# Kernel optimization log

Hardware: AMD Instinct MI355X
Metric: run time of the kernel (lower is better)

## Reference

```python
import jax, jax.numpy as jnp
import numpy as np

# config (matches init_kwargs)
B, L, Q = 4, 2048, 2048      # batch, memory_length, query_len
H, D = 16, 64                # heads, head_dim
E = H * D                    # hidden_dim = 1024
NB = 512                     # num_basis
SIGMAS = np.array([0.005, 0.01])
RIDGE = 0.5
CLAMP_MIN = 1e-4


def _build_basis():
    # torch.meshgrid(linspace(0,1,NB//2), sigmas) then flatten: mu repeated, sigma tiled
    mu = np.repeat(np.linspace(0.0, 1.0, NB // len(SIGMAS)), len(SIGMAS))
    sg = np.tile(SIGMAS, NB // len(SIGMAS))
    return mu, sg


def _build_G(mu, sg):
    # get_positions(L, padding=True), L even: 2L points in [-0.5+shift, 1.5-shift]
    shift = 1.0 / (2 * L)
    pos = np.linspace(-0.5 + shift, 1.5 - shift, 2 * L)
    # F[j, p] = N(pos_p; mu_j, sg_j)
    Fm = np.exp(-0.5 * ((pos[None, :] - mu[:, None]) / sg[:, None]) ** 2) / (sg[:, None] * np.sqrt(2 * np.pi))
    G = Fm.T @ np.linalg.inv(Fm @ Fm.T + RIDGE * np.eye(NB))  # [2L, NB]
    return G[L // 2:-(L // 2)]  # [L, NB]


def setup_inputs() -> dict:
    key = jax.random.key(0)
    ks = jax.random.split(key, 8)
    mu, sg = _build_basis()
    G = _build_G(mu, sg)
    s_e = 1.0 / np.sqrt(E)
    s_n = 1.0 / np.sqrt(NB)
    return {
        "k": jax.random.normal(ks[0], (B, L, E), jnp.float32),
        "q": jax.random.normal(ks[1], (B, Q, E), jnp.float32),
        "Wq": jax.random.normal(ks[2], (E, E), jnp.float32) * s_e,
        "Wk": jax.random.normal(ks[3], (E, E), jnp.float32) * s_e,
        "Wv": jax.random.normal(ks[4], (E, E), jnp.float32) * s_e,
        "Wo": jax.random.normal(ks[5], (E, E), jnp.float32) * s_e,
        "w_mu": jax.random.normal(ks[6], (NB,), jnp.float32) * s_n,
        "w_sigma": jax.random.normal(ks[7], (NB,), jnp.float32) * s_n,
        "Gs": jnp.asarray(G, jnp.float32),
        "basis_mu": jnp.asarray(mu, jnp.float32),
        "basis_sigma": jnp.asarray(sg, jnp.float32),
    }


def reference(k, q, Wq, Wk, Wv, Wo, w_mu, w_sigma, Gs, basis_mu, basis_sigma):
    # continuous compression of the memory: B_mat[b,n,e] = sum_l k[b,l,e] * Gs[l,n]
    Bm = jnp.einsum('ble,ln->bne', k, Gs)  # [B, NB, E]
    keys = (Bm @ Wk.T).reshape(B, NB, H, D).transpose(0, 2, 1, 3)   # [B,H,NB,D]
    vals = (Bm @ Wv.T).reshape(B, NB, H, D).transpose(0, 2, 1, 3)   # [B,H,NB,D]
    qry = (q @ Wq.T).reshape(B, Q, H, D).transpose(0, 2, 1, 3)      # [B,H,Q,D]
    # scores over basis functions
    scores = jnp.einsum('bhqd,bhnd->bhqn', qry, keys) / jnp.sqrt(jnp.float32(D))
    # affine heads -> Gaussian attention density parameters per query
    mu_q = jax.nn.sigmoid(scores @ w_mu)[..., None]                         # [B,H,Q,1]
    sig2 = jnp.clip(jax.nn.softplus(scores @ w_sigma), CLAMP_MIN)[..., None]  # [B,H,Q,1]
    # continuous softmax closed form: r_j = N(mu_q; basis_mu_j, sig2 + basis_sigma_j^2)
    var = sig2 + basis_sigma ** 2                                           # [B,H,Q,NB]
    r = jnp.exp(-0.5 * (mu_q - basis_mu) ** 2 / var) / jnp.sqrt(2.0 * jnp.pi * var)
    ctx = jnp.einsum('bhqn,bhnd->bhqd', r, vals)                            # [B,H,Q,D]
    ctx = ctx.transpose(0, 2, 1, 3).reshape(B, Q, E)
    return ctx @ Wo.T
```

## Files before the change

kernel.cpp:

```cpp
#include <hip/hip_runtime.h>

#define BB 4
#define LL 2048
#define QQ 2048
#define HH 16
#define DD 64
#define EE 1024
#define NB 512

typedef __attribute__((ext_vector_type(8))) short bf16x8;
typedef __attribute__((ext_vector_type(4))) float f32x4;

__device__ inline ushort bf16_rne(float f) {
  uint u = __float_as_uint(f);
  return (ushort)((u + 0x7fffu + ((u >> 16) & 1u)) >> 16);
}
__device__ inline float bf16_f(ushort h) { return __uint_as_float((uint)h << 16); }
__device__ inline void hilo(float x, ushort& h, ushort& l) {
  h = bf16_rne(x);
  l = bf16_rne(x - bf16_f(h));
}

__device__ inline void cvt8_pack(const float* a, uint4& ph, uint4& pl) {
  ushort h[8], l[8];
  #pragma unroll
  for (int j = 0; j < 8; j++) hilo(a[j], h[j], l[j]);
  ph = make_uint4((uint)h[0] | ((uint)h[1] << 16), (uint)h[2] | ((uint)h[3] << 16),
                  (uint)h[4] | ((uint)h[5] << 16), (uint)h[6] | ((uint)h[7] << 16));
  pl = make_uint4((uint)l[0] | ((uint)l[1] << 16), (uint)l[2] | ((uint)l[3] << 16),
                  (uint)l[4] | ((uint)l[5] << 16), (uint)l[6] | ((uint)l[7] << 16));
}

__device__ inline void xcd_remap(int& bx, int& by, int& bz) {
  int gx = gridDim.x, gy = gridDim.y;
  int nwg = gx * gy * (int)gridDim.z;
  int lin = blockIdx.x + gx * (blockIdx.y + gy * blockIdx.z);
  int swz = (lin & 7) * (nwg >> 3) + (lin >> 3);
  bx = swz % gx; int tmp = swz / gx; by = tmp % gy; bz = tmp / gy;
}

__global__ __launch_bounds__(256) void cvt_hilo(
    const float* __restrict__ x, ushort* __restrict__ hi, ushort* __restrict__ lo, long n)
{
  long i0 = ((long)blockIdx.x * 256 + threadIdx.x) * 8;
  long stride = (long)gridDim.x * 2048;
  for (long i = i0; i < n; i += stride) {
    float a[8];
    *(float4*)&a[0] = *(const float4*)&x[i];
    *(float4*)&a[4] = *(const float4*)&x[i + 4];
    uint4 ph, pl;
    cvt8_pack(a, ph, pl);
    *(uint4*)&hi[i] = ph;
    *(uint4*)&lo[i] = pl;
  }
}

__global__ __launch_bounds__(256) void cvt_hilo2(
    const float* __restrict__ x0, ushort* __restrict__ h0, ushort* __restrict__ l0,
    const float* __restrict__ x1, ushort* __restrict__ h1, ushort* __restrict__ l1, long n)
{
  const float* x = blockIdx.y ? x1 : x0;
  ushort* hi = blockIdx.y ? h1 : h0;
  ushort* lo = blockIdx.y ? l1 : l0;
  long i0 = ((long)blockIdx.x * 256 + threadIdx.x) * 8;
  long stride = (long)gridDim.x * 2048;
  for (long i = i0; i < n; i += stride) {
    float a[8];
    *(float4*)&a[0] = *(const float4*)&x[i];
    *(float4*)&a[4] = *(const float4*)&x[i + 4];
    uint4 ph, pl;
    cvt8_pack(a, ph, pl);
    *(uint4*)&hi[i] = ph;
    *(uint4*)&lo[i] = pl;
  }
}

__global__ __launch_bounds__(256) void cvt_hiloT(
    const float* __restrict__ x, ushort* __restrict__ hiT, ushort* __restrict__ loT,
    int R, int C, long zIn, long zOut)
{
  x += (long)blockIdx.z * zIn; hiT += (long)blockIdx.z * zOut; loT += (long)blockIdx.z * zOut;
  __shared__ float tile[32][33];
  const int t = threadIdx.x;
  const long r0 = (long)blockIdx.y * 32, c0 = (long)blockIdx.x * 32;
  {
    int row = t >> 3, c4 = t & 7;
    float4 v = *(const float4*)&x[(r0 + row) * C + c0 + c4 * 4];
    tile[row][c4*4+0] = v.x; tile[row][c4*4+1] = v.y;
    tile[row][c4*4+2] = v.z; tile[row][c4*4+3] = v.w;
  }
  __syncthreads();
  {
    int col = t >> 3, r4 = t & 7;
    ushort h[4], l[4];
    #pragma unroll
    for (int j = 0; j < 4; j++) hilo(tile[r4 * 4 + j][col], h[j], l[j]);
    uint2 ph = make_uint2((uint)h[0] | ((uint)h[1] << 16), (uint)h[2] | ((uint)h[3] << 16));
    uint2 pl = make_uint2((uint)l[0] | ((uint)l[1] << 16), (uint)l[2] | ((uint)l[3] << 16));
    long o = (c0 + col) * (long)R + r0 + r4 * 4;
    *(uint2*)&hiT[o] = ph;
    *(uint2*)&loT[o] = pl;
  }
}

__global__ __launch_bounds__(256) void add_pairs(
    float* __restrict__ dst, long dstStride,
    const float* __restrict__ src, long srcPairStride, long n)
{
  float* d = dst + (long)blockIdx.z * dstStride;
  const float* s0 = src + (long)blockIdx.z * srcPairStride;
  const float* s1 = s0 + n;
  long i0 = ((long)blockIdx.x * 256 + threadIdx.x) * 4;
  long stride = (long)gridDim.x * 1024;
  for (long i = i0; i < n; i += stride) {
    float4 a = *(const float4*)&s0[i];
    float4 b = *(const float4*)&s1[i];
    a.x += b.x; a.y += b.y; a.z += b.z; a.w += b.w;
    *(float4*)&d[i] = a;
  }
}


__global__ __launch_bounds__(256) void gemm_nt128(
    const float* __restrict__ A, const float* __restrict__ B, float* __restrict__ C,
    int N, int K, long sA, long sB, long sC, int NS, int Kc)
{
  const int z = blockIdx.z;
  const int b = z / NS, ks = z - b * NS;
  A += (long)b * sA + (long)ks * Kc;
  B += (long)b * sB + (long)ks * Kc;
  C += (long)z * sC;
  __shared__ float As[32][132], Bs[32][132];
  const int t = threadIdx.x;
  const int tx = t & 15, ty = t >> 4;
  const long m0 = (long)blockIdx.y * 128, n0 = (long)blockIdx.x * 128;
  float acc[8][8] = {};
  for (int k0 = 0; k0 < Kc; k0 += 32) {
    #pragma unroll
    for (int i = 0; i < 4; i++) {
      int f = t + i * 256;
      int r = f >> 3, k4 = f & 7;
      float4 va = *(const float4*)&A[(m0 + r) * K + k0 + k4 * 4];
      As[k4*4+0][r] = va.x; As[k4*4+1][r] = va.y; As[k4*4+2][r] = va.z; As[k4*4+3][r] = va.w;
      float4 vb = *(const float4*)&B[(n0 + r) * K + k0 + k4 * 4];
      Bs[k4*4+0][r] = vb.x; Bs[k4*4+1][r] = vb.y; Bs[k4*4+2][r] = vb.z; Bs[k4*4+3][r] = vb.w;
    }
    __syncthreads();
    #pragma unroll
    for (int kk = 0; kk < 32; kk++) {
      float4 a0 = *(const float4*)&As[kk][ty*8];
      float4 a1 = *(const float4*)&As[kk][ty*8+4];
      float4 b0 = *(const float4*)&Bs[kk][tx*8];
      float4 b1 = *(const float4*)&Bs[kk][tx*8+4];
      float ar[8] = {a0.x,a0.y,a0.z,a0.w,a1.x,a1.y,a1.z,a1.w};
      float br[8] = {b0.x,b0.y,b0.z,b0.w,b1.x,b1.y,b1.z,b1.w};
      #pragma unroll
      for (int i = 0; i < 8; i++)
        #pragma unroll
        for (int j = 0; j < 8; j++)
          acc[i][j] += ar[i] * br[j];
    }
    __syncthreads();
  }
  #pragma unroll
  for (int i = 0; i < 8; i++) {
    float4 o0 = make_float4(acc[i][0], acc[i][1], acc[i][2], acc[i][3]);
    float4 o1 = make_float4(acc[i][4], acc[i][5], acc[i][6], acc[i][7]);
    *(float4*)&C[(m0 + ty*8 + i) * N + n0 + tx*8    ] = o0;
    *(float4*)&C[(m0 + ty*8 + i) * N + n0 + tx*8 + 4] = o1;
  }
}

__global__ __launch_bounds__(256) void gemm_tn128(
    const float* __restrict__ A, const float* __restrict__ B, float* __restrict__ C,
    int M, int N, long sA, long sB, long sC, int NS, int Kc)
{
  const int z = blockIdx.z;
  const int b = z / NS, ks = z - b * NS;
  A += (long)b * sA + (long)ks * Kc * M;
  B += (long)b * sB + (long)ks * Kc * N;
  C += (long)z * sC;
  __shared__ float As[32][132], Bs[32][132];
  const int t = threadIdx.x;
  const int tx = t & 15, ty = t >> 4;
  const long m0 = (long)blockIdx.y * 128, n0 = (long)blockIdx.x * 128;
  float acc[8][8] = {};
  for (int k0 = 0; k0 < Kc; k0 += 32) {
    #pragma unroll
    for (int i = 0; i < 4; i++) {
      int f = t + i * 256;
      int r = f >> 5, c4 = f & 31;
      *(float4*)&As[r][c4 * 4] = *(const float4*)&A[(long)(k0 + r) * M + m0 + c4 * 4];
      *(float4*)&Bs[r][c4 * 4] = *(const float4*)&B[(long)(k0 + r) * N + n0 + c4 * 4];
    }
    __syncthreads();
    #pragma unroll
    for (int kk = 0; kk < 32; kk++) {
      float4 a0 = *(const float4*)&As[kk][ty*8];
      float4 a1 = *(const float4*)&As[kk][ty*8+4];
      float4 b0 = *(const float4*)&Bs[kk][tx*8];
      float4 b1 = *(const float4*)&Bs[kk][tx*8+4];
      float ar[8] = {a0.x,a0.y,a0.z,a0.w,a1.x,a1.y,a1.z,a1.w};
      float br[8] = {b0.x,b0.y,b0.z,b0.w,b1.x,b1.y,b1.z,b1.w};
      #pragma unroll
      for (int i = 0; i < 8; i++)
        #pragma unroll
        for (int j = 0; j < 8; j++)
          acc[i][j] += ar[i] * br[j];
    }
    __syncthreads();
  }
  #pragma unroll
  for (int i = 0; i < 8; i++) {
    float4 o0 = make_float4(acc[i][0], acc[i][1], acc[i][2], acc[i][3]);
    float4 o1 = make_float4(acc[i][4], acc[i][5], acc[i][6], acc[i][7]);
    *(float4*)&C[(m0 + ty*8 + i) * N + n0 + tx*8    ] = o0;
    *(float4*)&C[(m0 + ty*8 + i) * N + n0 + tx*8 + 4] = o1;
  }
}

__global__ __launch_bounds__(256) void gemm_nt64(
    const float* __restrict__ A, const float* __restrict__ B, float* __restrict__ C,
    int M, int N, int K, long sA, long sB, long sC)
{
  A += (long)blockIdx.z * sA; B += (long)blockIdx.z * sB; C += (long)blockIdx.z * sC;
  __shared__ float As[32][68], Bs[32][68];
  const int t = threadIdx.x;
  const int tx = t & 15, ty = t >> 4;
  const int m0 = blockIdx.y * 64, n0 = blockIdx.x * 64;
  float acc[4][4] = {};
  for (int k0 = 0; k0 < K; k0 += 32) {
    #pragma unroll
    for (int i = 0; i < 2; i++) {
      int f = t + i * 256;
      int r = f >> 3, k4 = f & 7;
      float4 va = *(const float4*)&A[(long)(m0 + r) * K + k0 + k4 * 4];
      As[k4*4+0][r] = va.x; As[k4*4+1][r] = va.y; As[k4*4+2][r] = va.z; As[k4*4+3][r] = va.w;
      float4 vb = *(const float4*)&B[(long)(n0 + r) * K + k0 + k4 * 4];
      Bs[k4*4+0][r] = vb.x; Bs[k4*4+1][r] = vb.y; Bs[k4*4+2][r] = vb.z; Bs[k4*4+3][r] = vb.w;
    }
    __syncthreads();
    #pragma unroll
    for (int kk = 0; kk < 32; kk++) {
      float4 a4 = *(const float4*)&As[kk][ty * 4];
      float4 b4 = *(const float4*)&Bs[kk][tx * 4];
      float ar[4] = {a4.x, a4.y, a4.z, a4.w};
      float br[4] = {b4.x, b4.y, b4.z, b4.w};
      #pragma unroll
      for (int i = 0; i < 4; i++)
        #pragma unroll
        for (int j = 0; j < 4; j++)
          acc[i][j] += ar[i] * br[j];
    }
    __syncthreads();
  }
  #pragma unroll
  for (int i = 0; i < 4; i++) {
    float4 o = make_float4(acc[i][0], acc[i][1], acc[i][2], acc[i][3]);
    *(float4*)&C[(long)(m0 + ty*4 + i) * N + n0 + tx*4] = o;
  }
}


__global__ __launch_bounds__(256) void gemm_nt128_b3(
    const ushort* __restrict__ Ah, const ushort* __restrict__ Al,
    const ushort* __restrict__ Bh, const ushort* __restrict__ Bl,
    float* __restrict__ C, int N, int K, long sA, long sC, int NS, int Kc)
{
  int bx, by, bz;
  xcd_remap(bx, by, bz);
  const int zb = bz / NS, ks = bz - zb * NS;
  Ah += (long)zb * sA + (long)ks * Kc;
  Al += (long)zb * sA + (long)ks * Kc;
  Bh += (long)ks * Kc;
  Bl += (long)ks * Kc;
  C  += (long)bz * sC;
  __shared__ ushort AhS[4096], AlS[4096], BhS[4096], BlS[4096];
  const int t = threadIdx.x;
  const int l = t & 63, w = t >> 6;
  const long m0 = (long)by * 128, n0 = (long)bx * 128;
  const int frA = (w & 1) * 4;
  const int frB = (w >> 1) * 4;
  const int rs = ((((l & 15) ^ ((l >> 4) << 1)) + 16 * (l >> 4))) * 8;
  f32x4 acc[4][4] = {};
  for (int k0 = 0; k0 < Kc; k0 += 32) {
    #pragma unroll
    for (int p = 0; p < 2; p++) {
      int t2 = t + p * 256;
      int row = t2 >> 2, kq = t2 & 3;
      long goff = (m0 + row) * (long)K + k0 + kq * 8;
      long gofB = (n0 + row) * (long)K + k0 + kq * 8;
      int dst = (row >> 4) * 512 + ((((row & 15) ^ (kq << 1)) + 16 * kq)) * 8;
      *(uint4*)&AhS[dst] = *(const uint4*)(Ah + goff);
      *(uint4*)&AlS[dst] = *(const uint4*)(Al + goff);
      *(uint4*)&BhS[dst] = *(const uint4*)(Bh + gofB);
      *(uint4*)&BlS[dst] = *(const uint4*)(Bl + gofB);
    }
    __syncthreads();
    bf16x8 ah[4], al[4], bh[4], bl[4];
    #pragma unroll
    for (int i = 0; i < 4; i++) {
      ah[i] = *(const bf16x8*)&AhS[(frA + i) * 512 + rs];
      al[i] = *(const bf16x8*)&AlS[(frA + i) * 512 + rs];
      bh[i] = *(const bf16x8*)&BhS[(frB + i) * 512 + rs];
      bl[i] = *(const bf16x8*)&BlS[(frB + i) * 512 + rs];
    }
    #pragma unroll
    for (int i = 0; i < 4; i++)
      #pragma unroll
      for (int j = 0; j < 4; j++) {
        acc[i][j] = __builtin_amdgcn_mfma_f32_16x16x32_bf16(ah[i], bh[j], acc[i][j], 0, 0, 0);
        acc[i][j] = __builtin_amdgcn_mfma_f32_16x16x32_bf16(ah[i], bl[j], acc[i][j], 0, 0, 0);
        acc[i][j] = __builtin_amdgcn_mfma_f32_16x16x32_bf16(al[i], bh[j], acc[i][j], 0, 0, 0);
      }
    __syncthreads();
  }
  const long rbase = m0 + (w & 1) * 64 + (l >> 4) * 4;
  const int  cbase = (int)n0 + (w >> 1) * 64 + (l & 15);
  #pragma unroll
  for (int i = 0; i < 4; i++)
    #pragma unroll
    for (int j = 0; j < 4; j++)
      #pragma unroll
      for (int r = 0; r < 4; r++)
        C[(rbase + i * 16 + r) * N + cbase + j * 16] = acc[i][j][r];
}

__global__ __launch_bounds__(256) void gemm_nt64x128_b3(
    const ushort* __restrict__ Ah, const ushort* __restrict__ Al,
    const ushort* __restrict__ Bh, const ushort* __restrict__ Bl,
    float* __restrict__ C, int N, int K, long sB, long sC)
{
  int bx, by, bz;
  xcd_remap(bx, by, bz);
  Bh += (long)bz * sB; Bl += (long)bz * sB; C += (long)bz * sC;
  __shared__ ushort AhS[2048], AlS[2048], BhS[4096], BlS[4096];
  const int t = threadIdx.x;
  const int l = t & 63, w = t >> 6;
  const long m0 = (long)by * 64, n0 = (long)bx * 128;
  const int wm = w & 1, wn = w >> 1;
  const int rs = ((((l & 15) ^ ((l >> 4) << 1)) + 16 * (l >> 4))) * 8;
  f32x4 acc[2][4] = {};
  for (int k0 = 0; k0 < K; k0 += 32) {
    {
      int row = t >> 2, kq = t & 3;
      long goff = (m0 + row) * (long)K + k0 + kq * 8;
      int dst = (row >> 4) * 512 + ((((row & 15) ^ (kq << 1)) + 16 * kq)) * 8;
      *(uint4*)&AhS[dst] = *(const uint4*)(Ah + goff);
      *(uint4*)&AlS[dst] = *(const uint4*)(Al + goff);
    }
    #pragma unroll
    for (int p = 0; p < 2; p++) {
      int t2 = t + p * 256;
      int row = t2 >> 2, kq = t2 & 3;
      long gofB = (n0 + row) * (long)K + k0 + kq * 8;
      int dst = (row >> 4) * 512 + ((((row & 15) ^ (kq << 1)) + 16 * kq)) * 8;
      *(uint4*)&BhS[dst] = *(const uint4*)(Bh + gofB);
      *(uint4*)&BlS[dst] = *(const uint4*)(Bl + gofB);
    }
    __syncthreads();
    bf16x8 ah[2], al[2], bh[4], bl[4];
    #pragma unroll
    for (int i = 0; i < 2; i++) {
      ah[i] = *(const bf16x8*)&AhS[(wm * 2 + i) * 512 + rs];
      al[i] = *(const bf16x8*)&AlS[(wm * 2 + i) * 512 + rs];
    }
    #pragma unroll
    for (int j = 0; j < 4; j++) {
      bh[j] = *(const bf16x8*)&BhS[(wn * 4 + j) * 512 + rs];
      bl[j] = *(const bf16x8*)&BlS[(wn * 4 + j) * 512 + rs];
    }
    #pragma unroll
    for (int i = 0; i < 2; i++)
      #pragma unroll
      for (int j = 0; j < 4; j++) {
        acc[i][j] = __builtin_amdgcn_mfma_f32_16x16x32_bf16(ah[i], bh[j], acc[i][j], 0, 0, 0);
        acc[i][j] = __builtin_amdgcn_mfma_f32_16x16x32_bf16(ah[i], bl[j], acc[i][j], 0, 0, 0);
        acc[i][j] = __builtin_amdgcn_mfma_f32_16x16x32_bf16(al[i], bh[j], acc[i][j], 0, 0, 0);
      }
    __syncthreads();
  }
  const long rbase = m0 + wm * 32 + (l >> 4) * 4;
  const int  cbase = (int)n0 + wn * 64 + (l & 15);
  #pragma unroll
  for (int i = 0; i < 2; i++)
    #pragma unroll
    for (int j = 0; j < 4; j++)
      #pragma unroll
      for (int r = 0; r < 4; r++)
        C[(rbase + i * 16 + r) * N + cbase + j * 16] = acc[i][j][r];
}

__global__ __launch_bounds__(256) void cvt_valsT(
    const float* __restrict__ valsP, ushort* __restrict__ vTh, ushort* __restrict__ vTl,
    long slabStride)
{
  const int c = blockIdx.x, h = blockIdx.y, b = blockIdx.z;
  const int t = threadIdx.x;
  __shared__ float tile[32][68];
  const float* s0 = valsP + (long)(2 * b) * slabStride;
  const float* s1 = s0 + slabStride;
  {
    int r = t >> 3, c8 = (t & 7) * 8;
    long g = (long)(c * 32 + r) * EE + h * 64 + c8;
    float4 a0 = *(const float4*)&s0[g];     float4 b0 = *(const float4*)&s1[g];
    float4 a1 = *(const float4*)&s0[g + 4]; float4 b1 = *(const float4*)&s1[g + 4];
    a0.x += b0.x; a0.y += b0.y; a0.z += b0.z; a0.w += b0.w;
    a1.x += b1.x; a1.y += b1.y; a1.z += b1.z; a1.w += b1.w;
    *(float4*)&tile[r][c8] = a0;
    *(float4*)&tile[r][c8 + 4] = a1;
  }
  __syncthreads();
  const int f = t >> 6, l = t & 63;
  const int d = f * 16 + (l & 15), kq = l >> 4;
  float a[8];
  #pragma unroll
  for (int e = 0; e < 8; e++) a[e] = tile[kq * 8 + e][d];
  uint4 ph, pl;
  cvt8_pack(a, ph, pl);
  long obase = (((long)(b * HH + h) * 16 + c) * 2048) + (long)t * 8;
  *(uint4*)&vTh[obase] = ph;
  *(uint4*)&vTl[obase] = pl;
}

__global__ __launch_bounds__(256) void nb_ctx_mf(
    const ushort* __restrict__ vTh, const ushort* __restrict__ vTl,
    const float* __restrict__ muq, const float* __restrict__ sg2,
    const float* __restrict__ bmu, const float* __restrict__ bsg,
    ushort* __restrict__ ctxh, ushort* __restrict__ ctxl,
    long sMu, long sC)
{
  int bx, by, bz;
  xcd_remap(bx, by, bz);
  const int h = by, b = bz;
  const long q0 = (long)bx * 128;
  const int t = threadIdx.x;
  const int l = t & 63, w = t >> 6, wm = w & 1, wn = w >> 1;
  __shared__ ushort AhS[4096], AlS[4096];
  __shared__ ushort BhS[2048], BlS[2048];
  __shared__ float mu_s[128], s2_s[128], bm_s[NB], bv_s[NB];
  const float* muqb = muq + (long)b * sMu;
  const float* sg2b = sg2 + (long)b * sMu;
  if (t < 128) {
    mu_s[t] = muqb[(long)h * QQ + q0 + t];
    s2_s[t] = sg2b[(long)h * QQ + q0 + t];
  }
  for (int i = t; i < NB; i += 256) {
    bm_s[i] = bmu[i];
    float x = bsg[i];
    bv_s[i] = x * x;
  }
  __syncthreads();
  const ushort* vThb = vTh + ((long)(b * HH + h) * 16) * 2048;
  const ushort* vTlb = vTl + ((long)(b * HH + h) * 16) * 2048;
  f32x4 acc[4][2] = {};
  for (int c = 0; c < 16; c++) {
    ((uint4*)BhS)[t] = ((const uint4*)(vThb + c * 2048))[t];
    ((uint4*)BlS)[t] = ((const uint4*)(vTlb + c * 2048))[t];
    #pragma unroll
    for (int p = 0; p < 2; p++) {
      int s = t + p * 256;
      int lf = s & 63;
      int q = ((s >> 6) << 4) + (lf & 15);
      int nb = c * 32 + (lf >> 4) * 8;
      float m = mu_s[q], s2 = s2_s[q];
      float a[8];
      #pragma unroll
      for (int e = 0; e < 8; e++) {
        float v = s2 + bv_s[nb + e];
        float d = m - bm_s[nb + e];
        float rv = __builtin_amdgcn_rcpf(v);
        a[e] = __expf(d * d * rv * -0.5f) * __builtin_amdgcn_rsqf(v * 6.2831853071795865f);
      }
      uint4 ph, pl;
      cvt8_pack(a, ph, pl);
      *(uint4*)&AhS[s * 8] = ph;
      *(uint4*)&AlS[s * 8] = pl;
    }
    __syncthreads();
    bf16x8 bhf[2], blf[2];
    #pragma unroll
    for (int j = 0; j < 2; j++) {
      bhf[j] = *(const bf16x8*)&BhS[(wn * 2 + j) * 512 + l * 8];
      blf[j] = *(const bf16x8*)&BlS[(wn * 2 + j) * 512 + l * 8];
    }
    #pragma unroll
    for (int i = 0; i < 4; i++) {
      bf16x8 ah = *(const bf16x8*)&AhS[(wm * 4 + i) * 512 + l * 8];
      bf16x8 al = *(const bf16x8*)&AlS[(wm * 4 + i) * 512 + l * 8];
      #pragma unroll
      for (int j = 0; j < 2; j++) {
        acc[i][j] = __builtin_amdgcn_mfma_f32_16x16x32_bf16(ah, bhf[j], acc[i][j], 0, 0, 0);
        acc[i][j] = __builtin_amdgcn_mfma_f32_16x16x32_bf16(ah, blf[j], acc[i][j], 0, 0, 0);
        acc[i][j] = __builtin_amdgcn_mfma_f32_16x16x32_bf16(al, bhf[j], acc[i][j], 0, 0, 0);
      }
    }
    __syncthreads();
  }
  ushort* ch = ctxh + (long)b * sC;
  ushort* cl = ctxl + (long)b * sC;
  const long rbase = q0 + wm * 64 + (l >> 4) * 4;
  const int  cbase = h * 64 + wn * 32 + (l & 15);
  #pragma unroll
  for (int i = 0; i < 4; i++)
    #pragma unroll
    for (int j = 0; j < 2; j++)
      #pragma unroll
      for (int r = 0; r < 4; r++) {
        long off = (rbase + i * 16 + r) * EE + cbase + j * 16;
        ushort hb, lb;
        hilo(acc[i][j][r], hb, lb);
        ch[off] = hb;
        cl[off] = lb;
      }
}

__global__ __launch_bounds__(256) void nb_uvec(
    const float* __restrict__ Bm, const float* __restrict__ wmu, const float* __restrict__ wsg,
    float* __restrict__ ump, float* __restrict__ usp, long sBm, long sU)
{
  Bm += (long)blockIdx.z * sBm; ump += (long)blockIdx.z * sU; usp += (long)blockIdx.z * sU;
  const int e = blockIdx.x * 256 + threadIdx.x;
  const int c = blockIdx.y;
  float am = 0.f, as = 0.f;
  #pragma unroll 8
  for (int n = c * 64; n < c * 64 + 64; n++) {
    float bv = Bm[(long)n * EE + e];
    am += wmu[n] * bv;
    as += wsg[n] * bv;
  }
  ump[(long)c * EE + e] = am;
  usp[(long)c * EE + e] = as;
}

__global__ __launch_bounds__(256) void nb_kw(
    const float* __restrict__ Wk, const float* __restrict__ ump, const float* __restrict__ usp,
    float* __restrict__ kwm, float* __restrict__ kws, long sU, long sK)
{
  ump += (long)blockIdx.z * sU; usp += (long)blockIdx.z * sU;
  kwm += (long)blockIdx.z * sK; kws += (long)blockIdx.z * sK;
  __shared__ float pm[256], ps[256];
  const int e = blockIdx.x, t = threadIdx.x;
  const float* row = Wk + (long)e * EE;
  float am = 0.f, as = 0.f;
  for (int i = t; i < EE; i += 256) {
    float um = 0.f, us = 0.f;
    #pragma unroll
    for (int c = 0; c < 8; c++) { um += ump[(long)c * EE + i]; us += usp[(long)c * EE + i]; }
    float w = row[i];
    am += w * um;
    as += w * us;
  }
  pm[t] = am; ps[t] = as;
  __syncthreads();
  for (int s = 128; s > 0; s >>= 1) {
    if (t < s) { pm[t] += pm[t + s]; ps[t] += ps[t + s]; }
    __syncthreads();
  }
  if (t == 0) { kwm[e] = pm[0]; kws[e] = ps[0]; }
}

__global__ __launch_bounds__(256) void nb_amas(
    const float* __restrict__ Wq, const float* __restrict__ kwm, const float* __restrict__ kws,
    float* __restrict__ AmAs, long sK, long sAm)
{
  kwm += (long)blockIdx.z * sK; kws += (long)blockIdx.z * sK;
  AmAs += (long)blockIdx.z * sAm;
  __shared__ float km[64], ks[64];
  const int t = threadIdx.x;
  const int h = blockIdx.y;
  const int e = blockIdx.x * 256 + t;
  if (t < 64) { km[t] = kwm[h * 64 + t]; ks[t] = kws[h * 64 + t]; }
  __syncthreads();
  float am = 0.f, as = 0.f;
  #pragma unroll 8
  for (int d = 0; d < 64; d++) {
    float w = Wq[(long)(h * 64 + d) * EE + e];
    am += km[d] * w;
    as += ks[d] * w;
  }
  AmAs[(long)e * 32 + h]      = am;
  AmAs[(long)e * 32 + 16 + h] = as;
}

__global__ __launch_bounds__(256) void nb_musig8(
    const float* __restrict__ qb, const float* __restrict__ AmAs,
    float* __restrict__ muq, float* __restrict__ sg2, long sQ, long sAm, long sMu)
{
  qb += (long)blockIdx.z * sQ; AmAs += (long)blockIdx.z * sAm;
  muq += (long)blockIdx.z * sMu; sg2 += (long)blockIdx.z * sMu;
  __shared__ float qs[8 * EE];
  const int t = threadIdx.x;
  const long q0 = (long)blockIdx.x * 8;
  for (int i = t * 4; i < 8 * EE; i += 1024)
    *(float4*)&qs[i] = *(const float4*)&qb[q0 * EE + i];
  __syncthreads();
  const int o = t & 31, row = t >> 5;
  const float* qr = qs + row * EE;
  float acc = 0.f;
  #pragma unroll 8
  for (int e = 0; e < EE; e++)
    acc += qr[e] * AmAs[(long)e * 32 + o];
  float s = acc * 0.125f;
  if (o < 16) {
    muq[(long)o * QQ + q0 + row] = 1.f / (1.f + expf(-s));
  } else {
    float sp = (s > 20.f) ? s : log1pf(expf(s));
    sg2[(long)(o - 16) * QQ + q0 + row] = fmaxf(sp, 1e-4f);
  }
}

__global__ __launch_bounds__(256) void nb_musig(
    const float* __restrict__ qb, const float* __restrict__ AmAs,
    float* __restrict__ muq, float* __restrict__ sg2, long sQ, long sAm, long sMu)
{
  qb += (long)blockIdx.z * sQ; AmAs += (long)blockIdx.z * sAm;
  muq += (long)blockIdx.z * sMu; sg2 += (long)blockIdx.z * sMu;
  __shared__ float qs[EE];
  __shared__ float part[8][32];
  const int t = threadIdx.x, qrow = blockIdx.x;
  for (int i = t; i < EE; i += 256) qs[i] = qb[(long)qrow * EE + i];
  __syncthreads();
  const int o = t & 31, ch = t >> 5;
  float acc = 0.f;
  const int e0 = ch * 128;
  #pragma unroll 8
  for (int i = 0; i < 128; i++) {
    int e = e0 + i;
    acc += qs[e] * AmAs[(long)e * 32 + o];
  }
  part[ch][o] = acc;
  __syncthreads();
  if (t < 32) {
    float s = 0.f;
    #pragma unroll
    for (int c = 0; c < 8; c++) s += part[c][o];
    s *= 0.125f;
    if (o < 16) {
      muq[(long)o * QQ + qrow] = 1.f / (1.f + expf(-s));
    } else {
      float sp = (s > 20.f) ? s : log1pf(expf(s));
      sg2[(long)(o - 16) * QQ + qrow] = fmaxf(sp, 1e-4f);
    }
  }
}

__global__ __launch_bounds__(128) void nb_ctx128(
    const float* __restrict__ vals, const float* __restrict__ muq, const float* __restrict__ sg2,
    const float* __restrict__ bmu,  const float* __restrict__ bsg, float* __restrict__ ctx,
    long sV, long sMu, long sC)
{
  vals += (long)blockIdx.z * sV; ctx += (long)blockIdx.z * sC;
  muq += (long)blockIdx.z * sMu; sg2 += (long)blockIdx.z * sMu;
  __shared__ float As[32][132], Bs[32][68];
  __shared__ __align__(16) float mu_s[128], s2_s[128];
  const int t = threadIdx.x;
  const int tx = t & 7, ty = t >> 3;
  const long q0 = (long)blockIdx.x * 128;
  const int h = blockIdx.y;
  mu_s[t] = muq[(long)h * QQ + q0 + t];
  s2_s[t] = sg2[(long)h * QQ + q0 + t];
  __syncthreads();
  float acc[8][8] = {};
  for (int n0 = 0; n0 < NB; n0 += 32) {
    #pragma unroll
    for (int i = 0; i < 4; i++) {
      int f = t + i * 128;
      int r = f >> 4, c4 = f & 15;
      *(float4*)&Bs[r][c4 * 4] = *(const float4*)&vals[(long)(n0 + r) * EE + h * 64 + c4 * 4];
    }
    #pragma unroll
    for (int i = 0; i < 8; i++) {
      int idx = t + i * 128;
      int n = idx >> 5, qg = idx & 31;
      float bm = bmu[n0 + n], bs = bsg[n0 + n];
      float bs2 = bs * bs;
      float4 m4 = *(const float4*)&mu_s[qg * 4];
      float4 s4 = *(const float4*)&s2_s[qg * 4];
      float4 rr;
      {
        float v0 = s4.x + bs2, d0 = m4.x - bm;
        float v1 = s4.y + bs2, d1 = m4.y - bm;
        float v2 = s4.z + bs2, d2 = m4.z - bm;
        float v3 = s4.w + bs2, d3 = m4.w - bm;
        float r0 = __builtin_amdgcn_rcpf(v0), r1 = __builtin_amdgcn_rcpf(v1);
        float r2 = __builtin_amdgcn_rcpf(v2), r3 = __builtin_amdgcn_rcpf(v3);
        rr.x = __expf(d0 * d0 * r0 * -0.5f) * __builtin_amdgcn_rsqf(v0 * 6.2831853071795865f);
        rr.y = __expf(d1 * d1 * r1 * -0.5f) * __builtin_amdgcn_rsqf(v1 * 6.2831853071795865f);
        rr.z = __expf(d2 * d2 * r2 * -0.5f) * __builtin_amdgcn_rsqf(v2 * 6.2831853071795865f);
        rr.w = __expf(d3 * d3 * r3 * -0.5f) * __builtin_amdgcn_rsqf(v3 * 6.2831853071795865f);
      }
      *(float4*)&As[n][qg * 4] = rr;
    }
    __syncthreads();
    #pragma unroll
    for (int kk = 0; kk < 32; kk++) {
      float4 a0 = *(const float4*)&As[kk][ty*8];
      float4 a1 = *(const float4*)&As[kk][ty*8+4];
      float4 b0 = *(const float4*)&Bs[kk][tx*8];
      float4 b1 = *(const float4*)&Bs[kk][tx*8+4];
      float ar[8] = {a0.x,a0.y,a0.z,a0.w,a1.x,a1.y,a1.z,a1.w};
      float br[8] = {b0.x,b0.y,b0.z,b0.w,b1.x,b1.y,b1.z,b1.w};
      #pragma unroll
      for (int i = 0; i < 8; i++)
        #pragma unroll
        for (int j = 0; j < 8; j++)
          acc[i][j] += ar[i] * br[j];
    }
    __syncthreads();
  }
  #pragma unroll
  for (int i = 0; i < 8; i++) {
    float4 o0 = make_float4(acc[i][0], acc[i][1], acc[i][2], acc[i][3]);
    float4 o1 = make_float4(acc[i][4], acc[i][5], acc[i][6], acc[i][7]);
    *(float4*)&ctx[(q0 + ty*8 + i) * EE + h * 64 + tx*8    ] = o0;
    *(float4*)&ctx[(q0 + ty*8 + i) * EE + h * 64 + tx*8 + 4] = o1;
  }
}

extern "C" void kernel_launch(void* const* d_in, const int* in_sizes, int n_in,
                              void* d_out, int out_size, void* d_ws, size_t ws_size,
                              hipStream_t stream) {
  const float* k   = (const float*)d_in[0];
  const float* q   = (const float*)d_in[1];
  const float* Wq  = (const float*)d_in[2];
  const float* Wk  = (const float*)d_in[3];
  const float* Wv  = (const float*)d_in[4];
  const float* Wo  = (const float*)d_in[5];
  const float* wmu = (const float*)d_in[6];
  const float* wsg = (const float*)d_in[7];
  const float* Gs  = (const float*)d_in[8];
  const float* bmu = (const float*)d_in[9];
  const float* bsg = (const float*)d_in[10];
  float* out = (float*)d_out;
  char* ws = (char*)d_ws;

  const long sBm = (long)NB * EE;
  const long sU  = 8L * EE;
  const long sK  = EE;
  const long sAm = 32L * EE;
  const long sMu = (long)HH * QQ;
  const long sQ  = (long)QQ * EE;

  if (ws_size >= (50u << 20)) {
    ushort* kTh  = (ushort*)(ws + 0);
    ushort* kTl  = (ushort*)(ws + (16u << 20));
    ushort* GsTh = (ushort*)(ws + (32u << 20));
    ushort* GsTl = (ushort*)(ws + (34u << 20));
    float*  Bm4  = (float*)(ws + (40u << 20));
    ushort* Bmh  = (ushort*)(ws + 0);
    ushort* Bml  = (ushort*)(ws + (4u << 20));
    ushort* Wvh  = (ushort*)(ws + (8u << 20));
    ushort* Wvl  = (ushort*)(ws + (10u << 20));
    float*  valsP= (float*)(ws + (16u << 20));
    ushort* vTh  = (ushort*)(ws + (32u << 20));
    ushort* vTl  = (ushort*)(ws + (36u << 20));
    ushort* Woh  = (ushort*)(ws + (40u << 20));
    ushort* Wol  = (ushort*)(ws + (42u << 20));
    ushort* ctxh = (ushort*)(ws + 0);
    ushort* ctxl = (ushort*)(ws + (16u << 20));
    char*  sm    = ws + (48u << 20);
    float* ump4  = (float*)(sm);
    float* usp4  = (float*)(sm + (128u << 10));
    float* kwm4  = (float*)(sm + (256u << 10));
    float* kws4  = (float*)(sm + (272u << 10));
    float* AmAs4 = (float*)(sm + (288u << 10));
    float* muq4  = (float*)(sm + (800u << 10));
    float* sg24  = (float*)(sm + (1312u << 10));

    cvt_hiloT<<<dim3(NB/32, LL/32, 1),  256, 0, stream>>>(Gs, GsTh, GsTl, LL, NB, 0L, 0L);
    cvt_hiloT<<<dim3(EE/32, LL/32, BB), 256, 0, stream>>>(k, kTh, kTl, LL, EE,
                                                          (long)LL*EE, (long)LL*EE);
    gemm_nt64x128_b3<<<dim3(EE/128, NB/64, BB), 256, 0, stream>>>(
        GsTh, GsTl, kTh, kTl, Bm4, EE, LL, (long)LL*EE, sBm);
    nb_uvec  <<<dim3(EE/256, 8, BB),  256, 0, stream>>>(Bm4, wmu, wsg, ump4, usp4, sBm, sU);
    nb_kw    <<<dim3(EE, 1, BB),      256, 0, stream>>>(Wk, ump4, usp4, kwm4, kws4, sU, sK);
    nb_amas  <<<dim3(EE/256, HH, BB), 256, 0, stream>>>(Wq, kwm4, kws4, AmAs4, sK, sAm);
    nb_musig8<<<dim3(QQ/8, 1, BB),    256, 0, stream>>>(q, AmAs4, muq4, sg24, sQ, sAm, sMu);
    cvt_hilo<<<dim3(256), 256, 0, stream>>>(Bm4, Bmh, Bml, (long)BB * sBm);
    cvt_hilo2<<<dim3(128, 2), 256, 0, stream>>>(Wv, Wvh, Wvl, Wo, Woh, Wol, (long)EE * EE);
    gemm_nt128_b3<<<dim3(EE/128, NB/128, BB*2), 256, 0, stream>>>(
        Bmh, Bml, Wvh, Wvl, valsP, EE, EE, sBm, sBm, 2, EE/2);
    cvt_valsT<<<dim3(16, HH, BB), 256, 0, stream>>>(valsP, vTh, vTl, sBm);
    nb_ctx_mf<<<dim3(QQ/128, HH, BB), 256, 0, stream>>>(
        vTh, vTl, muq4, sg24, bmu, bsg, ctxh, ctxl, sMu, sQ);
    gemm_nt128_b3<<<dim3(EE/128, QQ/128, BB), 256, 0, stream>>>(
        ctxh, ctxl, Woh, Wol, out, EE, EE, sQ, sQ, 1, EE);
  } else {
    float* BmP   = (float*)(ws + 0);
    float* ctxS  = (float*)(ws + 0);
    float* vals4 = (float*)(ws + (16u << 20));
    char*  sm    = ws + (24u << 20);
    float* ump4  = (float*)(sm);
    float* usp4  = (float*)(sm + (128u << 10));
    float* kwm4  = (float*)(sm + (256u << 10));
    float* kws4  = (float*)(sm + (272u << 10));
    float* AmAs4 = (float*)(sm + (288u << 10));
    float* muq4  = (float*)(sm + (800u << 10));
    float* sg24  = (float*)(sm + (1312u << 10));

    gemm_tn128<<<dim3(EE/128, NB/128, BB*2), 256, 0, stream>>>(
        Gs, k, BmP, NB, EE, 0L, (long)LL*EE, sBm, 2, LL/2);
    add_pairs<<<dim3(256, 1, BB), 256, 0, stream>>>(BmP, 2*sBm, BmP, 2*sBm, sBm);
    gemm_nt128<<<dim3(EE/128, NB/128, BB), 256, 0, stream>>>(
        BmP, Wv, vals4, EE, EE, 2*sBm, 0L, sBm, 1, EE);
    nb_uvec  <<<dim3(EE/256, 8, BB),  256, 0, stream>>>(BmP, wmu, wsg, ump4, usp4, 2*sBm, sU);
    nb_kw    <<<dim3(EE, 1, BB),      256, 0, stream>>>(Wk, ump4, usp4, kwm4, kws4, sU, sK);
    nb_amas  <<<dim3(EE/256, HH, BB), 256, 0, stream>>>(Wq, kwm4, kws4, AmAs4, sK, sAm);
    nb_musig <<<dim3(QQ, 1, BB),      256, 0, stream>>>(q, AmAs4, muq4, sg24, sQ, sAm, sMu);
    for (int b = 0; b < BB; b++) {
      nb_ctx128<<<dim3(QQ/128, HH, 1), 128, 0, stream>>>(
          vals4 + (long)b*sBm, muq4 + (long)b*sMu, sg24 + (long)b*sMu,
          bmu, bsg, ctxS, 0L, 0L, 0L);
      gemm_nt64<<<dim3(EE/64, QQ/64, 1), 256, 0, stream>>>(
          ctxS, Wo, out + (long)b*sQ, QQ, EE, EE, 0L, 0L, 0L);
    }
  }
  (void)in_sizes; (void)n_in; (void)out_size;
}
```

Before: 405.8 us.

## Emit hi/lo bf16 from GEMM epilogues and compute values transposed directly

```diff
diff --git a/kernel.cpp b/kernel.cpp
--- a/kernel.cpp
+++ b/kernel.cpp
@@ -12,8 +12,8 @@
 typedef __attribute__((ext_vector_type(4))) float f32x4;
 
 __device__ inline ushort bf16_rne(float f) {
-  uint u = __float_as_uint(f);
-  return (ushort)((u + 0x7fffu + ((u >> 16) & 1u)) >> 16);
+  __bf16 b = static_cast<__bf16>(f);
+  return __builtin_bit_cast(ushort, b);
 }
 __device__ inline float bf16_f(ushort h) { return __uint_as_float((uint)h << 16); }
 __device__ inline void hilo(float x, ushort& h, ushort& l) {
@@ -55,26 +55,6 @@
   }
 }
 
-__global__ __launch_bounds__(256) void cvt_hilo2(
-    const float* __restrict__ x0, ushort* __restrict__ h0, ushort* __restrict__ l0,
-    const float* __restrict__ x1, ushort* __restrict__ h1, ushort* __restrict__ l1, long n)
-{
-  const float* x = blockIdx.y ? x1 : x0;
-  ushort* hi = blockIdx.y ? h1 : h0;
-  ushort* lo = blockIdx.y ? l1 : l0;
-  long i0 = ((long)blockIdx.x * 256 + threadIdx.x) * 8;
-  long stride = (long)gridDim.x * 2048;
-  for (long i = i0; i < n; i += stride) {
-    float a[8];
-    *(float4*)&a[0] = *(const float4*)&x[i];
-    *(float4*)&a[4] = *(const float4*)&x[i + 4];
-    uint4 ph, pl;
-    cvt8_pack(a, ph, pl);
-    *(uint4*)&hi[i] = ph;
-    *(uint4*)&lo[i] = pl;
-  }
-}
-
 __global__ __launch_bounds__(256) void cvt_hiloT(
     const float* __restrict__ x, ushort* __restrict__ hiT, ushort* __restrict__ loT,
     int R, int C, long zIn, long zOut)
@@ -326,14 +306,15 @@
         C[(rbase + i * 16 + r) * N + cbase + j * 16] = acc[i][j][r];
 }
 
-__global__ __launch_bounds__(256) void gemm_nt64x128_b3(
+__global__ __launch_bounds__(256) void gemm_nt64x128_b3_us(
     const ushort* __restrict__ Ah, const ushort* __restrict__ Al,
     const ushort* __restrict__ Bh, const ushort* __restrict__ Bl,
-    float* __restrict__ C, int N, int K, long sB, long sC)
+    ushort* __restrict__ Ch, ushort* __restrict__ Cl, int N, int K, long sB, long sC)
 {
   int bx, by, bz;
   xcd_remap(bx, by, bz);
-  Bh += (long)bz * sB; Bl += (long)bz * sB; C += (long)bz * sC;
+  Bh += (long)bz * sB; Bl += (long)bz * sB;
+  Ch += (long)bz * sC; Cl += (long)bz * sC;
   __shared__ ushort AhS[2048], AlS[2048], BhS[4096], BlS[4096];
   const int t = threadIdx.x;
   const int l = t & 63, w = t >> 6;
@@ -387,40 +368,13 @@
     #pragma unroll
     for (int j = 0; j < 4; j++)
       #pragma unroll
-      for (int r = 0; r < 4; r++)
-        C[(rbase + i * 16 + r) * N + cbase + j * 16] = acc[i][j][r];
-}
-
-__global__ __launch_bounds__(256) void cvt_valsT(
-    const float* __restrict__ valsP, ushort* __restrict__ vTh, ushort* __restrict__ vTl,
-    long slabStride)
-{
-  const int c = blockIdx.x, h = blockIdx.y, b = blockIdx.z;
-  const int t = threadIdx.x;
-  __shared__ float tile[32][68];
-  const float* s0 = valsP + (long)(2 * b) * slabStride;
-  const float* s1 = s0 + slabStride;
-  {
-    int r = t >> 3, c8 = (t & 7) * 8;
-    long g = (long)(c * 32 + r) * EE + h * 64 + c8;
-    float4 a0 = *(const float4*)&s0[g];     float4 b0 = *(const float4*)&s1[g];
-    float4 a1 = *(const float4*)&s0[g + 4]; float4 b1 = *(const float4*)&s1[g + 4];
-    a0.x += b0.x; a0.y += b0.y; a0.z += b0.z; a0.w += b0.w;
-    a1.x += b1.x; a1.y += b1.y; a1.z += b1.z; a1.w += b1.w;
-    *(float4*)&tile[r][c8] = a0;
-    *(float4*)&tile[r][c8 + 4] = a1;
-  }
-  __syncthreads();
-  const int f = t >> 6, l = t & 63;
-  const int d = f * 16 + (l & 15), kq = l >> 4;
-  float a[8];
-  #pragma unroll
-  for (int e = 0; e < 8; e++) a[e] = tile[kq * 8 + e][d];
-  uint4 ph, pl;
-  cvt8_pack(a, ph, pl);
-  long obase = (((long)(b * HH + h) * 16 + c) * 2048) + (long)t * 8;
-  *(uint4*)&vTh[obase] = ph;
-  *(uint4*)&vTl[obase] = pl;
+      for (int r = 0; r < 4; r++) {
+        long off = (rbase + i * 16 + r) * N + cbase + j * 16;
+        ushort hb, lb;
+        hilo(acc[i][j][r], hb, lb);
+        Ch[off] = hb;
+        Cl[off] = lb;
+      }
 }
 
 __global__ __launch_bounds__(256) void nb_ctx_mf(
@@ -428,7 +382,7 @@
     const float* __restrict__ muq, const float* __restrict__ sg2,
     const float* __restrict__ bmu, const float* __restrict__ bsg,
     ushort* __restrict__ ctxh, ushort* __restrict__ ctxl,
-    long sMu, long sC)
+    long sMu, long sC, long sV)
 {
   int bx, by, bz;
   xcd_remap(bx, by, bz);
@@ -451,26 +405,31 @@
     bv_s[i] = x * x;
   }
   __syncthreads();
-  const ushort* vThb = vTh + ((long)(b * HH + h) * 16) * 2048;
-  const ushort* vTlb = vTl + ((long)(b * HH + h) * 16) * 2048;
+  const ushort* vThb = vTh + (long)b * sV + (long)(h * 64) * NB;
+  const ushort* vTlb = vTl + (long)b * sV + (long)(h * 64) * NB;
+  const int rs = ((((l & 15) ^ ((l >> 4) << 1)) + 16 * (l >> 4))) * 8;
+  const int srow = t >> 2, skq = t & 3;
+  const long bsrc = (long)srow * NB + skq * 8;
+  const int bdst = (srow >> 4) * 512 + ((((srow & 15) ^ (skq << 1)) + 16 * skq)) * 8;
   f32x4 acc[4][2] = {};
   for (int c = 0; c < 16; c++) {
-    ((uint4*)BhS)[t] = ((const uint4*)(vThb + c * 2048))[t];
-    ((uint4*)BlS)[t] = ((const uint4*)(vTlb + c * 2048))[t];
+    *(uint4*)&BhS[bdst] = *(const uint4*)(vThb + bsrc + c * 32);
+    *(uint4*)&BlS[bdst] = *(const uint4*)(vTlb + bsrc + c * 32);
     #pragma unroll
     for (int p = 0; p < 2; p++) {
       int s = t + p * 256;
       int lf = s & 63;
-      int q = ((s >> 6) << 4) + (lf & 15);
-      int nb = c * 32 + (lf >> 4) * 8;
-      float m = mu_s[q], s2 = s2_s[q];
+      int qq = ((s >> 6) << 4) + (lf & 15);
+      int nb0 = c * 32 + (lf >> 4) * 8;
+      float m = mu_s[qq], s2 = s2_s[qq];
       float a[8];
       #pragma unroll
       for (int e = 0; e < 8; e++) {
-        float v = s2 + bv_s[nb + e];
-        float d = m - bm_s[nb + e];
-        float rv = __builtin_amdgcn_rcpf(v);
-        a[e] = __expf(d * d * rv * -0.5f) * __builtin_amdgcn_rsqf(v * 6.2831853071795865f);
+        float v = s2 + bv_s[nb0 + e];
+        float d = m - bm_s[nb0 + e];
+        float si = __builtin_amdgcn_rsqf(v);
+        float tt = d * si;
+        a[e] = __expf(tt * tt * -0.5f) * (si * 0.3989422804014327f);
       }
       uint4 ph, pl;
       cvt8_pack(a, ph, pl);
@@ -481,8 +440,8 @@
     bf16x8 bhf[2], blf[2];
     #pragma unroll
     for (int j = 0; j < 2; j++) {
-      bhf[j] = *(const bf16x8*)&BhS[(wn * 2 + j) * 512 + l * 8];
-      blf[j] = *(const bf16x8*)&BlS[(wn * 2 + j) * 512 + l * 8];
+      bhf[j] = *(const bf16x8*)&BhS[(wn * 2 + j) * 512 + rs];
+      blf[j] = *(const bf16x8*)&BlS[(wn * 2 + j) * 512 + rs];
     }
     #pragma unroll
     for (int i = 0; i < 4; i++) {
@@ -513,6 +472,26 @@
         ch[off] = hb;
         cl[off] = lb;
       }
+}
+
+__global__ __launch_bounds__(256) void nb_uvec_us(
+    const ushort* __restrict__ Bmh, const ushort* __restrict__ Bml,
+    const float* __restrict__ wmu, const float* __restrict__ wsg,
+    float* __restrict__ ump, float* __restrict__ usp, long sBm, long sU)
+{
+  Bmh += (long)blockIdx.z * sBm; Bml += (long)blockIdx.z * sBm;
+  ump += (long)blockIdx.z * sU; usp += (long)blockIdx.z * sU;
+  const int e = blockIdx.x * 256 + threadIdx.x;
+  const int c = blockIdx.y;
+  float am = 0.f, as = 0.f;
+  #pragma unroll 8
+  for (int n = c * 64; n < c * 64 + 64; n++) {
+    float bv = bf16_f(Bmh[(long)n * EE + e]) + bf16_f(Bml[(long)n * EE + e]);
+    am += wmu[n] * bv;
+    as += wsg[n] * bv;
+  }
+  ump[(long)c * EE + e] = am;
+  usp[(long)c * EE + e] = as;
 }
 
 __global__ __launch_bounds__(256) void nb_uvec(
@@ -747,16 +726,14 @@
     ushort* kTl  = (ushort*)(ws + (16u << 20));
     ushort* GsTh = (ushort*)(ws + (32u << 20));
     ushort* GsTl = (ushort*)(ws + (34u << 20));
-    float*  Bm4  = (float*)(ws + (40u << 20));
-    ushort* Bmh  = (ushort*)(ws + 0);
-    ushort* Bml  = (ushort*)(ws + (4u << 20));
-    ushort* Wvh  = (ushort*)(ws + (8u << 20));
-    ushort* Wvl  = (ushort*)(ws + (10u << 20));
-    float*  valsP= (float*)(ws + (16u << 20));
+    ushort* Bmh  = (ushort*)(ws + (40u << 20));
+    ushort* Bml  = (ushort*)(ws + (44u << 20));
+    ushort* Wvh  = (ushort*)(ws + 0);
+    ushort* Wvl  = (ushort*)(ws + (2u << 20));
     ushort* vTh  = (ushort*)(ws + (32u << 20));
     ushort* vTl  = (ushort*)(ws + (36u << 20));
-    ushort* Woh  = (ushort*)(ws + (40u << 20));
-    ushort* Wol  = (ushort*)(ws + (42u << 20));
+    ushort* Woh  = (ushort*)(ws + (32u << 20));
+    ushort* Wol  = (ushort*)(ws + (34u << 20));
     ushort* ctxh = (ushort*)(ws + 0);
     ushort* ctxl = (ushort*)(ws + (16u << 20));
     char*  sm    = ws + (48u << 20);
@@ -771,19 +748,18 @@
     cvt_hiloT<<<dim3(NB/32, LL/32, 1),  256, 0, stream>>>(Gs, GsTh, GsTl, LL, NB, 0L, 0L);
     cvt_hiloT<<<dim3(EE/32, LL/32, BB), 256, 0, stream>>>(k, kTh, kTl, LL, EE,
                                                           (long)LL*EE, (long)LL*EE);
-    gemm_nt64x128_b3<<<dim3(EE/128, NB/64, BB), 256, 0, stream>>>(
-        GsTh, GsTl, kTh, kTl, Bm4, EE, LL, (long)LL*EE, sBm);
-    nb_uvec  <<<dim3(EE/256, 8, BB),  256, 0, stream>>>(Bm4, wmu, wsg, ump4, usp4, sBm, sU);
-    nb_kw    <<<dim3(EE, 1, BB),      256, 0, stream>>>(Wk, ump4, usp4, kwm4, kws4, sU, sK);
-    nb_amas  <<<dim3(EE/256, HH, BB), 256, 0, stream>>>(Wq, kwm4, kws4, AmAs4, sK, sAm);
-    nb_musig8<<<dim3(QQ/8, 1, BB),    256, 0, stream>>>(q, AmAs4, muq4, sg24, sQ, sAm, sMu);
-    cvt_hilo<<<dim3(256), 256, 0, stream>>>(Bm4, Bmh, Bml, (long)BB * sBm);
-    cvt_hilo2<<<dim3(128, 2), 256, 0, stream>>>(Wv, Wvh, Wvl, Wo, Woh, Wol, (long)EE * EE);
-    gemm_nt128_b3<<<dim3(EE/128, NB/128, BB*2), 256, 0, stream>>>(
-        Bmh, Bml, Wvh, Wvl, valsP, EE, EE, sBm, sBm, 2, EE/2);
-    cvt_valsT<<<dim3(16, HH, BB), 256, 0, stream>>>(valsP, vTh, vTl, sBm);
+    gemm_nt64x128_b3_us<<<dim3(EE/128, NB/64, BB), 256, 0, stream>>>(
+        GsTh, GsTl, kTh, kTl, Bmh, Bml, EE, LL, (long)LL*EE, sBm);
+    nb_uvec_us<<<dim3(EE/256, 8, BB),  256, 0, stream>>>(Bmh, Bml, wmu, wsg, ump4, usp4, sBm, sU);
+    nb_kw     <<<dim3(EE, 1, BB),      256, 0, stream>>>(Wk, ump4, usp4, kwm4, kws4, sU, sK);
+    nb_amas   <<<dim3(EE/256, HH, BB), 256, 0, stream>>>(Wq, kwm4, kws4, AmAs4, sK, sAm);
+    nb_musig8 <<<dim3(QQ/8, 1, BB),    256, 0, stream>>>(q, AmAs4, muq4, sg24, sQ, sAm, sMu);
+    cvt_hilo<<<dim3(256), 256, 0, stream>>>(Wv, Wvh, Wvl, (long)EE * EE);
+    gemm_nt64x128_b3_us<<<dim3(NB/128, EE/64, BB), 256, 0, stream>>>(
+        Wvh, Wvl, Bmh, Bml, vTh, vTl, NB, EE, sBm, sBm);
     nb_ctx_mf<<<dim3(QQ/128, HH, BB), 256, 0, stream>>>(
-        vTh, vTl, muq4, sg24, bmu, bsg, ctxh, ctxl, sMu, sQ);
+        vTh, vTl, muq4, sg24, bmu, bsg, ctxh, ctxl, sMu, sQ, sBm);
+    cvt_hilo<<<dim3(256), 256, 0, stream>>>(Wo, Woh, Wol, (long)EE * EE);
     gemm_nt128_b3<<<dim3(EE/128, QQ/128, BB), 256, 0, stream>>>(
         ctxh, ctxl, Woh, Wol, out, EE, EE, sQ, sQ, 1, EE);
   } else {
```

After: 392.2 us. -3.4%, faster.
